# Kernel tuning notes

Hardware: AMD Instinct MI355X
Metric: run time of the kernel (lower is better)

The kernel has to match this reference:

```python
import jax, jax.numpy as jnp
import numpy as np

EMB = 256
N_NODES = 20000
N_EDGES = 200000


def _sage_layer(x, src, dst, edge_attr, W, b, n_nodes):
    # message = x[src] + edge_attr ; mean-aggregate into dst ; ReLU(Linear([x;agg]))
    msg = x[src] + edge_attr                                   # [2E, emb]
    s = jax.ops.segment_sum(msg, dst, num_segments=n_nodes)    # [N, emb]
    cnt = jax.ops.segment_sum(jnp.ones((dst.shape[0], 1), x.dtype), dst,
                              num_segments=n_nodes)            # [N, 1]
    agg = s / jnp.maximum(cnt, 1.0)
    return jax.nn.relu(jnp.concatenate([x, agg], axis=1) @ W + b)


def setup_inputs() -> dict:
    key = jax.random.key(0)
    ks = jax.random.split(key, 12)
    sc = 0.05
    inp = {
        "x": jax.random.normal(ks[0], (N_NODES, EMB), jnp.float32),
        "edge_attr": jax.random.normal(ks[1], (N_EDGES, EMB), jnp.float32),
        "batch_q_embds": jax.random.normal(ks[2], (N_EDGES, EMB), jnp.float32),
        "edge_index": jax.random.randint(ks[3], (2, N_EDGES), 0, N_NODES, jnp.int64
                                         if jax.config.jax_enable_x64 else jnp.int32),
        "W_rev1": jax.random.normal(ks[4], (EMB, EMB), jnp.float32) * sc,
        "b_rev1": jnp.zeros((EMB,), jnp.float32),
        "W_rev2": jax.random.normal(ks[5], (EMB, EMB), jnp.float32) * sc,
        "b_rev2": jnp.zeros((EMB,), jnp.float32),
        "W_sage1": jax.random.normal(ks[6], (2 * EMB, EMB), jnp.float32) * sc,
        "b_sage1": jnp.zeros((EMB,), jnp.float32),
        "W_sage2": jax.random.normal(ks[7], (2 * EMB, EMB), jnp.float32) * sc,
        "b_sage2": jnp.zeros((EMB,), jnp.float32),
        "W_pred1": jax.random.normal(ks[8], (6 * EMB, EMB), jnp.float32) * sc,
        "b_pred1": jnp.zeros((EMB,), jnp.float32),
        "W_pred2": jax.random.normal(ks[9], (EMB, 1), jnp.float32) * sc,
        "b_pred2": jnp.zeros((1,), jnp.float32),
    }
    return inp


def reference(x, edge_attr, batch_q_embds, edge_index,
              W_rev1, b_rev1, W_rev2, b_rev2,
              W_sage1, b_sage1, W_sage2, b_sage2,
              W_pred1, b_pred1, W_pred2, b_pred2):
    src, dst = edge_index[0], edge_index[1]
    # reverse-edge attributes via proj_reverse MLP
    edge_attr_rev = jax.nn.relu(edge_attr @ W_rev1 + b_rev1) @ W_rev2 + b_rev2
    src_f = jnp.concatenate([src, dst])          # [2E]
    dst_f = jnp.concatenate([dst, src])          # [2E]
    ea_f = jnp.concatenate([edge_attr, edge_attr_rev], axis=0)  # [2E, emb]
    # 2-layer GraphSAGE backbone over nodes, collect per-layer outputs
    h1 = _sage_layer(x, src_f, dst_f, ea_f, W_sage1, b_sage1, N_NODES)
    h2 = _sage_layer(h1, src_f, dst_f, ea_f, W_sage2, b_sage2, N_NODES)
    h_e = jnp.concatenate([h1, h2], axis=1)      # [N, 2*emb]
    # per-edge triple features: [q ; h_e[head] ; edge_attr ; h_e[tail]]
    h_triple = jnp.concatenate([batch_q_embds, h_e[src], edge_attr, h_e[dst]], axis=1)
    attn_logits = (jax.nn.relu(h_triple @ W_pred1 + b_pred1) @ W_pred2 + b_pred2)[:, 0]
    # idp-bern sampling (training=True): gumbel-like logistic noise, temp=1
    u = jax.random.uniform(jax.random.key(42), attn_logits.shape,
                           attn_logits.dtype, 1e-10, 1.0 - 1e-10)
    noise = jnp.log(u) - jnp.log(1.0 - u)
    sampled = jax.nn.sigmoid(attn_logits + noise)
    return attn_logits, sampled
```

## Files before the change

kernel.cpp:

```cpp
#include <hip/hip_runtime.h>
#include <cstdint>
#include <cstddef>

#define EMB 256
#define NN 20000
#define NE 200000
#define NE2 400000

typedef unsigned short ushort_t;
typedef __attribute__((ext_vector_type(8))) short bf16x8;
typedef __attribute__((ext_vector_type(4))) float f32x4;

__device__ __forceinline__ ushort_t f2bf(float f) {
    unsigned u = __float_as_uint(f);
    u += 0x7FFFu + ((u >> 16) & 1u);
    return (ushort_t)(u >> 16);
}
__device__ __forceinline__ float bf2f(ushort_t u) {
    return __uint_as_float(((unsigned)u) << 16);
}

__device__ __forceinline__ void async_cp16(const ushort_t* g, ushort_t* l) {
    __builtin_amdgcn_global_load_lds(
        (const __attribute__((address_space(1))) unsigned int*)g,
        (__attribute__((address_space(3))) unsigned int*)l,
        16, 0, 0);
}

__device__ __forceinline__ unsigned rotl32(unsigned v, int d) {
    return (v << d) | (v >> (32 - d));
}
__device__ __forceinline__ void threefry2x32(unsigned k0, unsigned k1,
                                             unsigned x0, unsigned x1,
                                             unsigned& o0, unsigned& o1) {
    unsigned k2 = k0 ^ k1 ^ 0x1BD11BDAu;
    x0 += k0; x1 += k1;
#define TF_R(r) { x0 += x1; x1 = rotl32(x1, (r)); x1 ^= x0; }
    TF_R(13) TF_R(15) TF_R(26) TF_R(6)
    x0 += k1; x1 += k2 + 1u;
    TF_R(17) TF_R(29) TF_R(16) TF_R(24)
    x0 += k2; x1 += k0 + 2u;
    TF_R(13) TF_R(15) TF_R(26) TF_R(6)
    x0 += k0; x1 += k1 + 3u;
    TF_R(17) TF_R(29) TF_R(16) TF_R(24)
    x0 += k1; x1 += k2 + 4u;
    TF_R(13) TF_R(15) TF_R(26) TF_R(6)
    x0 += k2; x1 += k0 + 5u;
#undef TF_R
    o0 = x0; o1 = x1;
}

__global__ void deg_kernel(const int* __restrict__ src, const int* __restrict__ dst,
                           int* __restrict__ deg) {
    int i = blockIdx.x * blockDim.x + threadIdx.x;
    if (i < NE2) {
        int n = (i < NE) ? dst[i] : src[i - NE];
        atomicAdd(&deg[n], 1);
    }
}

__global__ void prefix_kernel(const int* __restrict__ deg, int* __restrict__ row_start,
                              int* __restrict__ cursor) {
    __shared__ int sums[1024];
    int t = threadIdx.x;
    const int CH = (NN + 1023) / 1024;
    int lo = t * CH, hi = lo + CH;
    if (hi > NN) hi = NN;
    if (lo > NN) lo = NN;
    int s = 0;
    for (int n = lo; n < hi; n++) s += deg[n];
    sums[t] = s;
    __syncthreads();
    for (int off = 1; off < 1024; off <<= 1) {
        int v = (t >= off) ? sums[t - off] : 0;
        __syncthreads();
        sums[t] += v;
        __syncthreads();
    }
    int run = (t == 0) ? 0 : sums[t - 1];
    for (int n = lo; n < hi; n++) {
        row_start[n] = run;
        cursor[n] = run;
        run += deg[n];
    }
    if (t == 1023) row_start[NN] = sums[1023];
}

__global__ void scatter_kernel(const int* __restrict__ src, const int* __restrict__ dst,
                               int* __restrict__ cursor, int* __restrict__ elist) {
    int i = blockIdx.x * blockDim.x + threadIdx.x;
    if (i < NE2) {
        int n = (i < NE) ? dst[i] : src[i - NE];
        int pos = atomicAdd(&cursor[n], 1);
        elist[pos] = i;
    }
}

__global__ void conv2_kernel(const float* __restrict__ a, ushort_t* __restrict__ oa, int na8,
                             const float* __restrict__ b, ushort_t* __restrict__ ob, int nb8) {
    int i = blockIdx.x * 256 + threadIdx.x;
    const float* p;
    ushort_t* o;
    if (i < na8) { p = a + (size_t)i * 8; o = oa + (size_t)i * 8; }
    else {
        int j = i - na8;
        if (j >= nb8) return;
        p = b + (size_t)j * 8; o = ob + (size_t)j * 8;
    }
    float4 u = *(const float4*)p;
    float4 v = *(const float4*)(p + 4);
    union { ushort_t s[8]; uint4 w; } r;
    r.s[0] = f2bf(u.x); r.s[1] = f2bf(u.y); r.s[2] = f2bf(u.z); r.s[3] = f2bf(u.w);
    r.s[4] = f2bf(v.x); r.s[5] = f2bf(v.y); r.s[6] = f2bf(v.z); r.s[7] = f2bf(v.w);
    *(uint4*)o = r.w;
}

struct TD { const float* src; ushort_t* dst; int stride, koff, kr; };
struct TA { TD d[8]; };

__global__ void transpose_all_kernel(TA ta) {
    TD t = ta.d[blockIdx.y];
    int k = blockIdx.x;
    if (k >= t.kr) return;
    int n = threadIdx.x;
    t.dst[(size_t)n * t.stride + t.koff + k] = f2bf(t.src[(size_t)k * 256 + n]);
}

template <int KTOT, int EPI, bool A0F32>
__global__ __launch_bounds__(256, 2) void mfma_gemm(
        const void* __restrict__ A0v, int rsA0,
        const ushort_t* __restrict__ A1, int rsA1,
        const ushort_t* __restrict__ Bt, const ushort_t* __restrict__ Bt2,
        const float* __restrict__ bias,
        void* __restrict__ out, void* __restrict__ out2, int rsOut, int M,
        const int* __restrict__ srcp, const int* __restrict__ dstp,
        const float* __restrict__ Hs, const float* __restrict__ Hd,
        const float* __restrict__ w2, const float* __restrict__ b2v,
        float* __restrict__ out_s) {
    __shared__ ushort_t As[128 * 32];
    __shared__ ushort_t Bs[256 * 32];
    __shared__ float red[128];

    int tid = threadIdx.x;
    int lane = tid & 63;
    int wave = tid >> 6;
    int wr = wave >> 1;
    int wc = wave & 1;
    int quad = lane >> 4;
    int col_l = lane & 15;
    int bm = blockIdx.x;

    const ushort_t* Bsel = blockIdx.y ? Bt2 : Bt;
    void* Osel = blockIdx.y ? out2 : out;

    f32x4 acc[4][8];
#pragma unroll
    for (int mt = 0; mt < 4; mt++)
#pragma unroll
        for (int nt = 0; nt < 8; nt++) acc[mt][nt] = (f32x4)0.f;

    for (int k0 = 0; k0 < KTOT; k0 += 32) {
        __syncthreads();
        bool seg1 = (KTOT == 512) && (k0 >= 256);
        if (A0F32 && !seg1) {
#pragma unroll
            for (int j = 0; j < 2; j++) {
                int flat = tid + 256 * j;
                int row = flat >> 2, ch = flat & 3;
                int grow = bm * 128 + row;
                if (grow >= M) grow = M - 1;
                const float* gp = (const float*)A0v + (size_t)grow * rsA0 + k0 + ch * 8;
                float4 u = *(const float4*)gp;
                float4 v = *(const float4*)(gp + 4);
                union { ushort_t s[8]; uint4 w; } r;
                r.s[0] = f2bf(u.x); r.s[1] = f2bf(u.y); r.s[2] = f2bf(u.z); r.s[3] = f2bf(u.w);
                r.s[4] = f2bf(v.x); r.s[5] = f2bf(v.y); r.s[6] = f2bf(v.z); r.s[7] = f2bf(v.w);
                *(uint4*)(As + (size_t)flat * 8) = r.w;
            }
        } else {
            const ushort_t* abase;
            int rs, koffs;
            if (seg1) { abase = A1; rs = rsA1; koffs = k0 - 256; }
            else      { abase = (const ushort_t*)A0v; rs = rsA0; koffs = k0; }
#pragma unroll
            for (int j = 0; j < 2; j++) {
                int flat = tid + 256 * j;
                int row = flat >> 2, ch = flat & 3;
                int grow = bm * 128 + row;
                if (grow >= M) grow = M - 1;
                const ushort_t* gp = abase + (size_t)grow * rs + koffs + ch * 8;
                ushort_t* lp = As + ((wave * 64 + 256 * j) * 8);
                async_cp16(gp, lp);
            }
        }
#pragma unroll
        for (int j = 0; j < 4; j++) {
            int flat = tid + 256 * j;
            int n = flat >> 2, ch = flat & 3;
            const ushort_t* gp = Bsel + (size_t)n * KTOT + k0 + ch * 8;
            ushort_t* lp = Bs + ((wave * 64 + 256 * j) * 8);
            async_cp16(gp, lp);
        }
        __syncthreads();

        bf16x8 a[4], b[8];
#pragma unroll
        for (int mt = 0; mt < 4; mt++)
            a[mt] = *(const bf16x8*)(As + (wr * 64 + mt * 16 + col_l) * 32 + quad * 8);
#pragma unroll
        for (int nt = 0; nt < 8; nt++)
            b[nt] = *(const bf16x8*)(Bs + (wc * 128 + nt * 16 + col_l) * 32 + quad * 8);
#pragma unroll
        for (int mt = 0; mt < 4; mt++)
#pragma unroll
            for (int nt = 0; nt < 8; nt++)
                acc[mt][nt] = __builtin_amdgcn_mfma_f32_16x16x32_bf16(
                    a[mt], b[nt], acc[mt][nt], 0, 0, 0);
    }

    if (EPI == 4) {
        if (tid < 128) red[tid] = 0.f;
        __syncthreads();
        float b1c[8], w2c[8];
#pragma unroll
        for (int nt = 0; nt < 8; nt++) {
            int col = wc * 128 + nt * 16 + col_l;
            b1c[nt] = bias[col];
            w2c[nt] = w2[col];
        }
#pragma unroll
        for (int mt = 0; mt < 4; mt++) {
#pragma unroll
            for (int r = 0; r < 4; r++) {
                int lrow = wr * 64 + mt * 16 + quad * 4 + r;
                int e = bm * 128 + lrow;
                int ec = e < M ? e : M - 1;
                int s = srcp[ec], d = dstp[ec];
                const float* hsr = Hs + (size_t)s * 256;
                const float* hdr = Hd + (size_t)d * 256;
                float part = 0.f;
#pragma unroll
                for (int nt = 0; nt < 8; nt++) {
                    int col = wc * 128 + nt * 16 + col_l;
                    part += fmaxf(acc[mt][nt][r] + hsr[col] + hdr[col] + b1c[nt], 0.f)
                            * w2c[nt];
                }
#pragma unroll
                for (int m = 8; m > 0; m >>= 1) part += __shfl_xor(part, m, 64);
                if (col_l == 0) atomicAdd(&red[lrow], part);
            }
        }
        __syncthreads();
        if (tid < 128) {
            int e = bm * 128 + tid;
            if (e < M) {
                float logit = red[tid] + b2v[0];
                ((float*)out)[e] = logit;
                unsigned y0, y1;
                threefry2x32(0u, 42u, 0u, (unsigned)e, y0, y1);
                unsigned bits = y0 ^ y1;
                float f = __uint_as_float((bits >> 9) | 0x3F800000u) - 1.0f;
                float u = fmaxf(1e-10f, f + 1e-10f);
                float noise = logf(u) - logf(1.0f - u);
                out_s[e] = 1.0f / (1.0f + expf(-(logit + noise)));
            }
        }
        return;
    }

    float bs[8];
    if (EPI >= 2) {
#pragma unroll
        for (int nt = 0; nt < 8; nt++) bs[nt] = bias[wc * 128 + nt * 16 + col_l];
    }
#pragma unroll
    for (int mt = 0; mt < 4; mt++) {
#pragma unroll
        for (int nt = 0; nt < 8; nt++) {
            int colg = wc * 128 + nt * 16 + col_l;
#pragma unroll
            for (int r = 0; r < 4; r++) {
                int rg = bm * 128 + wr * 64 + mt * 16 + quad * 4 + r;
                if (rg < M) {
                    float v = acc[mt][nt][r];
                    if (EPI >= 2) v += bs[nt];
                    if (EPI == 3) v = fmaxf(v, 0.f);
                    if (EPI == 0)
                        ((float*)Osel)[(size_t)rg * rsOut + colg] = v;
                    else
                        ((ushort_t*)Osel)[(size_t)rg * rsOut + colg] = f2bf(v);
                }
            }
        }
    }
}

__global__ __launch_bounds__(64) void agg_bf_kernel(
        const ushort_t* __restrict__ xin, int rsx,
        const ushort_t* __restrict__ eaf, const ushort_t* __restrict__ ear,
        const int* __restrict__ src, const int* __restrict__ dst,
        const int* __restrict__ row_start, const int* __restrict__ elist,
        const int* __restrict__ deg, ushort_t* __restrict__ agg) {
    int n = blockIdx.x;
    int c = threadIdx.x * 4;
    float ax = 0.f, ay = 0.f, az = 0.f, aw = 0.f;
    int beg = row_start[n], end = row_start[n + 1];
    for (int p = beg; p < end; p++) {
        int i = elist[p];
        const ushort_t* xr;
        const ushort_t* er;
        if (i < NE) { xr = xin + (size_t)src[i] * rsx; er = eaf + (size_t)i * 256; }
        else { int j = i - NE; xr = xin + (size_t)dst[j] * rsx; er = ear + (size_t)j * 256; }
        ushort4 xv = *(const ushort4*)(xr + c);
        ushort4 ev = *(const ushort4*)(er + c);
        ax += bf2f(xv.x) + bf2f(ev.x);
        ay += bf2f(xv.y) + bf2f(ev.y);
        az += bf2f(xv.z) + bf2f(ev.z);
        aw += bf2f(xv.w) + bf2f(ev.w);
    }
    float d = fmaxf((float)deg[n], 1.0f);
    ushort4 o;
    o.x = f2bf(ax / d); o.y = f2bf(ay / d); o.z = f2bf(az / d); o.w = f2bf(aw / d);
    *(ushort4*)(agg + (size_t)n * 256 + c) = o;
}

extern "C" void kernel_launch(void* const* d_in, const int* in_sizes, int n_in,
                              void* d_out, int out_size, void* d_ws, size_t ws_size,
                              hipStream_t stream) {
    const float* x        = (const float*)d_in[0];
    const float* ea       = (const float*)d_in[1];
    const float* qemb     = (const float*)d_in[2];
    const int*   eidx     = (const int*)d_in[3];
    const float* W_rev1   = (const float*)d_in[4];
    const float* b_rev1   = (const float*)d_in[5];
    const float* W_rev2   = (const float*)d_in[6];
    const float* b_rev2   = (const float*)d_in[7];
    const float* W_sage1  = (const float*)d_in[8];
    const float* b_sage1  = (const float*)d_in[9];
    const float* W_sage2  = (const float*)d_in[10];
    const float* b_sage2  = (const float*)d_in[11];
    const float* W_pred1  = (const float*)d_in[12];
    const float* b_pred1  = (const float*)d_in[13];
    const float* W_pred2  = (const float*)d_in[14];
    const float* b_pred2  = (const float*)d_in[15];
    float* out = (float*)d_out;

    const int* src = eidx;
    const int* dst = eidx + NE;

    char* w = (char*)d_ws;
    ushort_t* ea_bf  = (ushort_t*)w; w += (size_t)NE * 256 * 2;
    ushort_t* hid_bf = (ushort_t*)w; w += (size_t)NE * 256 * 2;
    ushort_t* ea_rev_bf = (ushort_t*)w; w += (size_t)NE * 256 * 2;
    ushort_t* x_bf   = (ushort_t*)w; w += (size_t)NN * 256 * 2;
    ushort_t* H      = (ushort_t*)w; w += (size_t)NN * 512 * 2;
    ushort_t* agg_bf = (ushort_t*)w; w += (size_t)NN * 256 * 2;
    float*    Hsrc   = (float*)w;    w += (size_t)NN * 256 * 4;
    float*    Hdst   = (float*)w;    w += (size_t)NN * 256 * 4;
    ushort_t* Wt_rev1  = (ushort_t*)w; w += 256 * 256 * 2;
    ushort_t* Wt_rev2  = (ushort_t*)w; w += 256 * 256 * 2;
    ushort_t* Wt_sage1 = (ushort_t*)w; w += 256 * 512 * 2;
    ushort_t* Wt_sage2 = (ushort_t*)w; w += 256 * 512 * 2;
    ushort_t* Wt_src   = (ushort_t*)w; w += 256 * 512 * 2;
    ushort_t* Wt_dst   = (ushort_t*)w; w += 256 * 512 * 2;
    ushort_t* Wt_edge  = (ushort_t*)w; w += 256 * 512 * 2;
    int* deg       = (int*)w; w += (size_t)NN * 4;
    int* row_start = (int*)w; w += (size_t)(NN + 1) * 4;
    int* cursor    = (int*)w; w += (size_t)NN * 4;
    int* elist     = (int*)w; w += (size_t)NE2 * 4;

    const int EB = (NE + 127) / 128;
    const int NB = (NN + 127) / 128;

    hipMemsetAsync(deg, 0, (size_t)NN * 4, stream);
    deg_kernel<<<(NE2 + 255) / 256, 256, 0, stream>>>(src, dst, deg);
    prefix_kernel<<<1, 1024, 0, stream>>>(deg, row_start, cursor);
    scatter_kernel<<<(NE2 + 255) / 256, 256, 0, stream>>>(src, dst, cursor, elist);

    TA ta;
    ta.d[0] = { W_rev1,  Wt_rev1,  256, 0,   256 };
    ta.d[1] = { W_rev2,  Wt_rev2,  256, 0,   256 };
    ta.d[2] = { W_sage1, Wt_sage1, 512, 0,   512 };
    ta.d[3] = { W_sage2, Wt_sage2, 512, 0,   512 };
    ta.d[4] = { W_pred1 + (size_t)256 * 256,  Wt_src,  512, 0,   512 };
    ta.d[5] = { W_pred1 + (size_t)1024 * 256, Wt_dst,  512, 0,   512 };
    ta.d[6] = { W_pred1,                      Wt_edge, 512, 0,   256 };
    ta.d[7] = { W_pred1 + (size_t)768 * 256,  Wt_edge, 512, 256, 256 };
    transpose_all_kernel<<<dim3(512, 8), 256, 0, stream>>>(ta);

    conv2_kernel<<<((NE + NN) * 32 + 255) / 256, 256, 0, stream>>>(
        ea, ea_bf, NE * 32, x, x_bf, NN * 32);

    mfma_gemm<256, 3, false><<<EB, 256, 0, stream>>>(
        ea_bf, 256, nullptr, 0, Wt_rev1, nullptr, b_rev1,
        hid_bf, nullptr, 256, NE, nullptr, nullptr, nullptr, nullptr, nullptr, nullptr, nullptr);
    mfma_gemm<256, 2, false><<<EB, 256, 0, stream>>>(
        hid_bf, 256, nullptr, 0, Wt_rev2, nullptr, b_rev2,
        ea_rev_bf, nullptr, 256, NE, nullptr, nullptr, nullptr, nullptr, nullptr, nullptr, nullptr);

    agg_bf_kernel<<<NN, 64, 0, stream>>>(x_bf, 256, ea_bf, ea_rev_bf,
                                         src, dst, row_start, elist, deg, agg_bf);
    mfma_gemm<512, 3, false><<<NB, 256, 0, stream>>>(
        x_bf, 256, agg_bf, 256, Wt_sage1, nullptr, b_sage1,
        H, nullptr, 512, NN, nullptr, nullptr, nullptr, nullptr, nullptr, nullptr, nullptr);

    agg_bf_kernel<<<NN, 64, 0, stream>>>(H, 512, ea_bf, ea_rev_bf,
                                         src, dst, row_start, elist, deg, agg_bf);
    mfma_gemm<512, 3, false><<<NB, 256, 0, stream>>>(
        H, 512, agg_bf, 256, Wt_sage2, nullptr, b_sage2,
        H + 256, nullptr, 512, NN, nullptr, nullptr, nullptr, nullptr, nullptr, nullptr, nullptr);

    mfma_gemm<512, 0, false><<<dim3(NB, 2), 256, 0, stream>>>(
        H, 512, H + 256, 512, Wt_src, Wt_dst, nullptr,
        Hsrc, Hdst, 256, NN, nullptr, nullptr, nullptr, nullptr, nullptr, nullptr, nullptr);

    mfma_gemm<512, 4, true><<<EB, 256, 0, stream>>>(
        qemb, 256, ea_bf, 256, Wt_edge, nullptr, b_pred1,
        out, nullptr, 0, NE, src, dst, Hsrc, Hdst, W_pred2, b_pred2, out + NE);
}
```

Before: 1.008 ms.

## Double-buffer LDS tiles in MFMA GEMM to overlap loads with compute

```diff
diff --git a/kernel.cpp b/kernel.cpp
--- a/kernel.cpp
+++ b/kernel.cpp
@@ -137,8 +137,8 @@
         const float* __restrict__ Hs, const float* __restrict__ Hd,
         const float* __restrict__ w2, const float* __restrict__ b2v,
         float* __restrict__ out_s) {
-    __shared__ ushort_t As[128 * 32];
-    __shared__ ushort_t Bs[256 * 32];
+    __shared__ ushort_t As[2][128 * 32];
+    __shared__ ushort_t Bs[2][256 * 32];
     __shared__ float red[128];
 
     int tid = threadIdx.x;
@@ -159,25 +159,33 @@
 #pragma unroll
         for (int nt = 0; nt < 8; nt++) acc[mt][nt] = (f32x4)0.f;
 
-    for (int k0 = 0; k0 < KTOT; k0 += 32) {
-        __syncthreads();
+    auto a0_load = [&](int k0, float4* u, float4* v) {
+#pragma unroll
+        for (int j = 0; j < 2; j++) {
+            int flat = tid + 256 * j;
+            int row = flat >> 2, ch = flat & 3;
+            int grow = bm * 128 + row;
+            if (grow >= M) grow = M - 1;
+            const float* gp = (const float*)A0v + (size_t)grow * rsA0 + k0 + ch * 8;
+            u[j] = *(const float4*)gp;
+            v[j] = *(const float4*)(gp + 4);
+        }
+    };
+    auto a0_write = [&](int buf, const float4* u, const float4* v) {
+#pragma unroll
+        for (int j = 0; j < 2; j++) {
+            int flat = tid + 256 * j;
+            union { ushort_t s[8]; uint4 w; } r;
+            r.s[0] = f2bf(u[j].x); r.s[1] = f2bf(u[j].y);
+            r.s[2] = f2bf(u[j].z); r.s[3] = f2bf(u[j].w);
+            r.s[4] = f2bf(v[j].x); r.s[5] = f2bf(v[j].y);
+            r.s[6] = f2bf(v[j].z); r.s[7] = f2bf(v[j].w);
+            *(uint4*)(&As[buf][(size_t)flat * 8]) = r.w;
+        }
+    };
+    auto stage = [&](int buf, int k0, bool skipA) {
         bool seg1 = (KTOT == 512) && (k0 >= 256);
-        if (A0F32 && !seg1) {
-#pragma unroll
-            for (int j = 0; j < 2; j++) {
-                int flat = tid + 256 * j;
-                int row = flat >> 2, ch = flat & 3;
-                int grow = bm * 128 + row;
-                if (grow >= M) grow = M - 1;
-                const float* gp = (const float*)A0v + (size_t)grow * rsA0 + k0 + ch * 8;
-                float4 u = *(const float4*)gp;
-                float4 v = *(const float4*)(gp + 4);
-                union { ushort_t s[8]; uint4 w; } r;
-                r.s[0] = f2bf(u.x); r.s[1] = f2bf(u.y); r.s[2] = f2bf(u.z); r.s[3] = f2bf(u.w);
-                r.s[4] = f2bf(v.x); r.s[5] = f2bf(v.y); r.s[6] = f2bf(v.z); r.s[7] = f2bf(v.w);
-                *(uint4*)(As + (size_t)flat * 8) = r.w;
-            }
-        } else {
+        if (!skipA) {
             const ushort_t* abase;
             int rs, koffs;
             if (seg1) { abase = A1; rs = rsA1; koffs = k0 - 256; }
@@ -189,7 +197,7 @@
                 int grow = bm * 128 + row;
                 if (grow >= M) grow = M - 1;
                 const ushort_t* gp = abase + (size_t)grow * rs + koffs + ch * 8;
-                ushort_t* lp = As + ((wave * 64 + 256 * j) * 8);
+                ushort_t* lp = &As[buf][(wave * 64 + 256 * j) * 8];
                 async_cp16(gp, lp);
             }
         }
@@ -198,24 +206,52 @@
             int flat = tid + 256 * j;
             int n = flat >> 2, ch = flat & 3;
             const ushort_t* gp = Bsel + (size_t)n * KTOT + k0 + ch * 8;
-            ushort_t* lp = Bs + ((wave * 64 + 256 * j) * 8);
+            ushort_t* lp = &Bs[buf][(wave * 64 + 256 * j) * 8];
             async_cp16(gp, lp);
         }
-        __syncthreads();
+    };
+
+    if (A0F32) {
+        float4 u0[2], v0[2];
+        a0_load(0, u0, v0);
+        stage(0, 0, true);
+        a0_write(0, u0, v0);
+    } else {
+        stage(0, 0, false);
+    }
+    __syncthreads();
+
+    const int NIT = KTOT / 32;
+    float4 pu[2], pv[2];
+#pragma unroll 2
+    for (int it = 0; it < NIT; ++it) {
+        int cur = it & 1;
+        int nxt = cur ^ 1;
+        int k1 = (it + 1) * 32;
+        bool do_pref = (it + 1 < NIT);
+        bool seg1_n = (KTOT == 512) && (k1 >= 256);
+        bool pref_f32 = A0F32 && do_pref && !seg1_n;
+
+        if (pref_f32) a0_load(k1, pu, pv);
+        if (do_pref) stage(nxt, k1, pref_f32);
 
         bf16x8 a[4], b[8];
 #pragma unroll
         for (int mt = 0; mt < 4; mt++)
-            a[mt] = *(const bf16x8*)(As + (wr * 64 + mt * 16 + col_l) * 32 + quad * 8);
+            a[mt] = *(const bf16x8*)(&As[cur][(wr * 64 + mt * 16 + col_l) * 32 + quad * 8]);
 #pragma unroll
         for (int nt = 0; nt < 8; nt++)
-            b[nt] = *(const bf16x8*)(Bs + (wc * 128 + nt * 16 + col_l) * 32 + quad * 8);
+            b[nt] = *(const bf16x8*)(&Bs[cur][(wc * 128 + nt * 16 + col_l) * 32 + quad * 8]);
 #pragma unroll
         for (int mt = 0; mt < 4; mt++)
 #pragma unroll
             for (int nt = 0; nt < 8; nt++)
                 acc[mt][nt] = __builtin_amdgcn_mfma_f32_16x16x32_bf16(
                     a[mt], b[nt], acc[mt][nt], 0, 0, 0);
+
+        if (pref_f32) a0_write(nxt, pu, pv);
+
+        __syncthreads();
     }
 
     if (EPI == 4) {
```

Measured after the change: 996.4 us. Within noise of the previous version (-1.2%).

## Triple-buffer GEMM LDS tiles with async prefetch; pre-convert query embeddings to bf16

Applied to the files above, without the earlier changes.

```diff
diff --git a/kernel.cpp b/kernel.cpp
--- a/kernel.cpp
+++ b/kernel.cpp
@@ -25,6 +25,13 @@
         (const __attribute__((address_space(1))) unsigned int*)g,
         (__attribute__((address_space(3))) unsigned int*)l,
         16, 0, 0);
+}
+
+__device__ __forceinline__ void waitbar6() {
+    asm volatile("s_waitcnt vmcnt(6) lgkmcnt(0)\n\ts_barrier" ::: "memory");
+}
+__device__ __forceinline__ void waitbar0() {
+    asm volatile("s_waitcnt vmcnt(0) lgkmcnt(0)\n\ts_barrier" ::: "memory");
 }
 
 __device__ __forceinline__ unsigned rotl32(unsigned v, int d) {
@@ -126,9 +133,9 @@
     t.dst[(size_t)n * t.stride + t.koff + k] = f2bf(t.src[(size_t)k * 256 + n]);
 }
 
-template <int KTOT, int EPI, bool A0F32>
+template <int KTOT, int EPI>
 __global__ __launch_bounds__(256, 2) void mfma_gemm(
-        const void* __restrict__ A0v, int rsA0,
+        const ushort_t* __restrict__ A0, int rsA0,
         const ushort_t* __restrict__ A1, int rsA1,
         const ushort_t* __restrict__ Bt, const ushort_t* __restrict__ Bt2,
         const float* __restrict__ bias,
@@ -137,8 +144,8 @@
         const float* __restrict__ Hs, const float* __restrict__ Hd,
         const float* __restrict__ w2, const float* __restrict__ b2v,
         float* __restrict__ out_s) {
-    __shared__ ushort_t As[128 * 32];
-    __shared__ ushort_t Bs[256 * 32];
+    __shared__ ushort_t As[3][128 * 32];
+    __shared__ ushort_t Bs[3][256 * 32];
     __shared__ float red[128];
 
     int tid = threadIdx.x;
@@ -159,66 +166,60 @@
 #pragma unroll
         for (int nt = 0; nt < 8; nt++) acc[mt][nt] = (f32x4)0.f;
 
-    for (int k0 = 0; k0 < KTOT; k0 += 32) {
-        __syncthreads();
-        bool seg1 = (KTOT == 512) && (k0 >= 256);
-        if (A0F32 && !seg1) {
-#pragma unroll
-            for (int j = 0; j < 2; j++) {
-                int flat = tid + 256 * j;
-                int row = flat >> 2, ch = flat & 3;
-                int grow = bm * 128 + row;
-                if (grow >= M) grow = M - 1;
-                const float* gp = (const float*)A0v + (size_t)grow * rsA0 + k0 + ch * 8;
-                float4 u = *(const float4*)gp;
-                float4 v = *(const float4*)(gp + 4);
-                union { ushort_t s[8]; uint4 w; } r;
-                r.s[0] = f2bf(u.x); r.s[1] = f2bf(u.y); r.s[2] = f2bf(u.z); r.s[3] = f2bf(u.w);
-                r.s[4] = f2bf(v.x); r.s[5] = f2bf(v.y); r.s[6] = f2bf(v.z); r.s[7] = f2bf(v.w);
-                *(uint4*)(As + (size_t)flat * 8) = r.w;
-            }
-        } else {
-            const ushort_t* abase;
-            int rs, koffs;
-            if (seg1) { abase = A1; rs = rsA1; koffs = k0 - 256; }
-            else      { abase = (const ushort_t*)A0v; rs = rsA0; koffs = k0; }
-#pragma unroll
-            for (int j = 0; j < 2; j++) {
-                int flat = tid + 256 * j;
-                int row = flat >> 2, ch = flat & 3;
-                int grow = bm * 128 + row;
-                if (grow >= M) grow = M - 1;
-                const ushort_t* gp = abase + (size_t)grow * rs + koffs + ch * 8;
-                ushort_t* lp = As + ((wave * 64 + 256 * j) * 8);
-                async_cp16(gp, lp);
-            }
+    auto stage = [&](int buf, int k0) {
+        const ushort_t* abase;
+        int rs, koffs;
+        if (KTOT == 512 && k0 >= 256) { abase = A1; rs = rsA1; koffs = k0 - 256; }
+        else                          { abase = A0; rs = rsA0; koffs = k0; }
+#pragma unroll
+        for (int j = 0; j < 2; j++) {
+            int flat = tid + 256 * j;
+            int row = flat >> 2, ch = flat & 3;
+            int grow = bm * 128 + row;
+            if (grow >= M) grow = M - 1;
+            const ushort_t* gp = abase + (size_t)grow * rs + koffs + ch * 8;
+            ushort_t* lp = &As[buf][(wave * 64 + 256 * j) * 8];
+            async_cp16(gp, lp);
         }
 #pragma unroll
         for (int j = 0; j < 4; j++) {
             int flat = tid + 256 * j;
             int n = flat >> 2, ch = flat & 3;
             const ushort_t* gp = Bsel + (size_t)n * KTOT + k0 + ch * 8;
-            ushort_t* lp = Bs + ((wave * 64 + 256 * j) * 8);
+            ushort_t* lp = &Bs[buf][(wave * 64 + 256 * j) * 8];
             async_cp16(gp, lp);
         }
-        __syncthreads();
-
+    };
+
+    auto compute = [&](int buf) {
         bf16x8 a[4], b[8];
 #pragma unroll
         for (int mt = 0; mt < 4; mt++)
-            a[mt] = *(const bf16x8*)(As + (wr * 64 + mt * 16 + col_l) * 32 + quad * 8);
+            a[mt] = *(const bf16x8*)(&As[buf][(wr * 64 + mt * 16 + col_l) * 32 + quad * 8]);
 #pragma unroll
         for (int nt = 0; nt < 8; nt++)
-            b[nt] = *(const bf16x8*)(Bs + (wc * 128 + nt * 16 + col_l) * 32 + quad * 8);
+            b[nt] = *(const bf16x8*)(&Bs[buf][(wc * 128 + nt * 16 + col_l) * 32 + quad * 8]);
 #pragma unroll
         for (int mt = 0; mt < 4; mt++)
 #pragma unroll
             for (int nt = 0; nt < 8; nt++)
                 acc[mt][nt] = __builtin_amdgcn_mfma_f32_16x16x32_bf16(
                     a[mt], b[nt], acc[mt][nt], 0, 0, 0);
-    }
+    };
+
+    const int NIT = KTOT / 32;
+    stage(0, 0);
+    stage(1, 32);
+    for (int k = 0; k < NIT - 1; ++k) {
+        waitbar6();
+        if (k + 2 < NIT) stage((k + 2) % 3, (k + 2) * 32);
+        compute(k % 3);
+    }
+    waitbar0();
+    compute((NIT - 1) % 3);
 
     if (EPI == 4) {
+        __syncthreads();
         if (tid < 128) red[tid] = 0.f;
         __syncthreads();
         float b1c[8], w2c[8];
@@ -391,30 +392,33 @@
     conv2_kernel<<<((NE + NN) * 32 + 255) / 256, 256, 0, stream>>>(
         ea, ea_bf, NE * 32, x, x_bf, NN * 32);
 
-    mfma_gemm<256, 3, false><<<EB, 256, 0, stream>>>(
+    mfma_gemm<256, 3><<<EB, 256, 0, stream>>>(
         ea_bf, 256, nullptr, 0, Wt_rev1, nullptr, b_rev1,
         hid_bf, nullptr, 256, NE, nullptr, nullptr, nullptr, nullptr, nullptr, nullptr, nullptr);
-    mfma_gemm<256, 2, false><<<EB, 256, 0, stream>>>(
+    mfma_gemm<256, 2><<<EB, 256, 0, stream>>>(
         hid_bf, 256, nullptr, 0, Wt_rev2, nullptr, b_rev2,
         ea_rev_bf, nullptr, 256, NE, nullptr, nullptr, nullptr, nullptr, nullptr, nullptr, nullptr);
 
+    conv2_kernel<<<(NE * 32 + 255) / 256, 256, 0, stream>>>(
+        qemb, hid_bf, NE * 32, qemb, hid_bf, 0);
+
     agg_bf_kernel<<<NN, 64, 0, stream>>>(x_bf, 256, ea_bf, ea_rev_bf,
                                          src, dst, row_start, elist, deg, agg_bf);
-    mfma_gemm<512, 3, false><<<NB, 256, 0, stream>>>(
+    mfma_gemm<512, 3><<<NB, 256, 0, stream>>>(
         x_bf, 256, agg_bf, 256, Wt_sage1, nullptr, b_sage1,
         H, nullptr, 512, NN, nullptr, nullptr, nullptr, nullptr, nullptr, nullptr, nullptr);
 
     agg_bf_kernel<<<NN, 64, 0, stream>>>(H, 512, ea_bf, ea_rev_bf,
                                          src, dst, row_start, elist, deg, agg_bf);
-    mfma_gemm<512, 3, false><<<NB, 256, 0, stream>>>(
+    mfma_gemm<512, 3><<<NB, 256, 0, stream>>>(
         H, 512, agg_bf, 256, Wt_sage2, nullptr, b_sage2,
         H + 256, nullptr, 512, NN, nullptr, nullptr, nullptr, nullptr, nullptr, nullptr, nullptr);
 
-    mfma_gemm<512, 0, false><<<dim3(NB, 2), 256, 0, stream>>>(
+    mfma_gemm<512, 0><<<dim3(NB, 2), 256, 0, stream>>>(
         H, 512, H + 256, 512, Wt_src, Wt_dst, nullptr,
         Hsrc, Hdst, 256, NN, nullptr, nullptr, nullptr, nullptr, nullptr, nullptr, nullptr);
 
-    mfma_gemm<512, 4, true><<<EB, 256, 0, stream>>>(
-        qemb, 256, ea_bf, 256, Wt_edge, nullptr, b_pred1,
+    mfma_gemm<512, 4><<<EB, 256, 0, stream>>>(
+        hid_bf, 256, ea_bf, 256, Wt_edge, nullptr, b_pred1,
         out, nullptr, 0, NE, src, dst, Hsrc, Hdst, W_pred2, b_pred2, out + NE);
 }
```

After: 1.086 ms. +7.7%, slower.

## Split GEMM output columns across two blocks and add separate finalize kernel

Applied to the files above, without the earlier changes.

```diff
diff --git a/kernel.cpp b/kernel.cpp
--- a/kernel.cpp
+++ b/kernel.cpp
@@ -126,19 +126,18 @@
     t.dst[(size_t)n * t.stride + t.koff + k] = f2bf(t.src[(size_t)k * 256 + n]);
 }
 
-template <int KTOT, int EPI, bool A0F32>
-__global__ __launch_bounds__(256, 2) void mfma_gemm(
-        const void* __restrict__ A0v, int rsA0,
+template <int KTOT, int EPI>
+__global__ __launch_bounds__(256, 3) void mfma_gemm(
+        const ushort_t* __restrict__ A0, int rsA0,
         const ushort_t* __restrict__ A1, int rsA1,
         const ushort_t* __restrict__ Bt, const ushort_t* __restrict__ Bt2,
         const float* __restrict__ bias,
         void* __restrict__ out, void* __restrict__ out2, int rsOut, int M,
         const int* __restrict__ srcp, const int* __restrict__ dstp,
         const float* __restrict__ Hs, const float* __restrict__ Hd,
-        const float* __restrict__ w2, const float* __restrict__ b2v,
-        float* __restrict__ out_s) {
+        const float* __restrict__ w2) {
     __shared__ ushort_t As[128 * 32];
-    __shared__ ushort_t Bs[256 * 32];
+    __shared__ ushort_t Bs[128 * 32];
     __shared__ float red[128];
 
     int tid = threadIdx.x;
@@ -148,83 +147,69 @@
     int wc = wave & 1;
     int quad = lane >> 4;
     int col_l = lane & 15;
-    int bm = blockIdx.x;
+    int p = blockIdx.x >> 1;
+    int colblk = blockIdx.x & 1;
 
     const ushort_t* Bsel = blockIdx.y ? Bt2 : Bt;
     void* Osel = blockIdx.y ? out2 : out;
 
-    f32x4 acc[4][8];
+    f32x4 acc[4][4];
 #pragma unroll
     for (int mt = 0; mt < 4; mt++)
 #pragma unroll
-        for (int nt = 0; nt < 8; nt++) acc[mt][nt] = (f32x4)0.f;
+        for (int nt = 0; nt < 4; nt++) acc[mt][nt] = (f32x4)0.f;
 
     for (int k0 = 0; k0 < KTOT; k0 += 32) {
         __syncthreads();
-        bool seg1 = (KTOT == 512) && (k0 >= 256);
-        if (A0F32 && !seg1) {
+        {
+            const ushort_t* abase;
+            int rs, koffs;
+            if (KTOT == 512 && k0 >= 256) { abase = A1; rs = rsA1; koffs = k0 - 256; }
+            else                          { abase = A0; rs = rsA0; koffs = k0; }
 #pragma unroll
             for (int j = 0; j < 2; j++) {
                 int flat = tid + 256 * j;
                 int row = flat >> 2, ch = flat & 3;
-                int grow = bm * 128 + row;
-                if (grow >= M) grow = M - 1;
-                const float* gp = (const float*)A0v + (size_t)grow * rsA0 + k0 + ch * 8;
-                float4 u = *(const float4*)gp;
-                float4 v = *(const float4*)(gp + 4);
-                union { ushort_t s[8]; uint4 w; } r;
-                r.s[0] = f2bf(u.x); r.s[1] = f2bf(u.y); r.s[2] = f2bf(u.z); r.s[3] = f2bf(u.w);
-                r.s[4] = f2bf(v.x); r.s[5] = f2bf(v.y); r.s[6] = f2bf(v.z); r.s[7] = f2bf(v.w);
-                *(uint4*)(As + (size_t)flat * 8) = r.w;
-            }
-        } else {
-            const ushort_t* abase;
-            int rs, koffs;
-            if (seg1) { abase = A1; rs = rsA1; koffs = k0 - 256; }
-            else      { abase = (const ushort_t*)A0v; rs = rsA0; koffs = k0; }
-#pragma unroll
-            for (int j = 0; j < 2; j++) {
-                int flat = tid + 256 * j;
-                int row = flat >> 2, ch = flat & 3;
-                int grow = bm * 128 + row;
+                int grow = p * 128 + row;
                 if (grow >= M) grow = M - 1;
                 const ushort_t* gp = abase + (size_t)grow * rs + koffs + ch * 8;
                 ushort_t* lp = As + ((wave * 64 + 256 * j) * 8);
                 async_cp16(gp, lp);
             }
+#pragma unroll
+            for (int j = 0; j < 2; j++) {
+                int flat = tid + 256 * j;
+                int n = flat >> 2, ch = flat & 3;
+                const ushort_t* gp = Bsel + (size_t)(colblk * 128 + n) * KTOT + k0 + ch * 8;
+                ushort_t* lp = Bs + ((wave * 64 + 256 * j) * 8);
+                async_cp16(gp, lp);
+            }
         }
-#pragma unroll
-        for (int j = 0; j < 4; j++) {
-            int flat = tid + 256 * j;
-            int n = flat >> 2, ch = flat & 3;
-            const ushort_t* gp = Bsel + (size_t)n * KTOT + k0 + ch * 8;
-            ushort_t* lp = Bs + ((wave * 64 + 256 * j) * 8);
-            async_cp16(gp, lp);
-        }
-        __syncthreads();
-
-        bf16x8 a[4], b[8];
+        __syncthreads();
+
+        bf16x8 a[4], b[4];
 #pragma unroll
         for (int mt = 0; mt < 4; mt++)
             a[mt] = *(const bf16x8*)(As + (wr * 64 + mt * 16 + col_l) * 32 + quad * 8);
 #pragma unroll
-        for (int nt = 0; nt < 8; nt++)
-            b[nt] = *(const bf16x8*)(Bs + (wc * 128 + nt * 16 + col_l) * 32 + quad * 8);
+        for (int nt = 0; nt < 4; nt++)
+            b[nt] = *(const bf16x8*)(Bs + (wc * 64 + nt * 16 + col_l) * 32 + quad * 8);
 #pragma unroll
         for (int mt = 0; mt < 4; mt++)
 #pragma unroll
-            for (int nt = 0; nt < 8; nt++)
+            for (int nt = 0; nt < 4; nt++)
                 acc[mt][nt] = __builtin_amdgcn_mfma_f32_16x16x32_bf16(
                     a[mt], b[nt], acc[mt][nt], 0, 0, 0);
     }
 
     if (EPI == 4) {
+        __syncthreads();
         if (tid < 128) red[tid] = 0.f;
         __syncthreads();
-        float b1c[8], w2c[8];
-#pragma unroll
-        for (int nt = 0; nt < 8; nt++) {
-            int col = wc * 128 + nt * 16 + col_l;
+        float b1c[4], w2c[4];
+#pragma unroll
+        for (int nt = 0; nt < 4; nt++) {
+            int col = colblk * 128 + wc * 64 + nt * 16 + col_l;
             b1c[nt] = bias[col];
             w2c[nt] = w2[col];
         }
@@ -233,15 +218,15 @@
 #pragma unroll
             for (int r = 0; r < 4; r++) {
                 int lrow = wr * 64 + mt * 16 + quad * 4 + r;
-                int e = bm * 128 + lrow;
+                int e = p * 128 + lrow;
                 int ec = e < M ? e : M - 1;
                 int s = srcp[ec], d = dstp[ec];
                 const float* hsr = Hs + (size_t)s * 256;
                 const float* hdr = Hd + (size_t)d * 256;
                 float part = 0.f;
 #pragma unroll
-                for (int nt = 0; nt < 8; nt++) {
-                    int col = wc * 128 + nt * 16 + col_l;
+                for (int nt = 0; nt < 4; nt++) {
+                    int col = colblk * 128 + wc * 64 + nt * 16 + col_l;
                     part += fmaxf(acc[mt][nt][r] + hsr[col] + hdr[col] + b1c[nt], 0.f)
                             * w2c[nt];
                 }
@@ -252,35 +237,29 @@
         }
         __syncthreads();
         if (tid < 128) {
-            int e = bm * 128 + tid;
+            int e = p * 128 + tid;
             if (e < M) {
-                float logit = red[tid] + b2v[0];
-                ((float*)out)[e] = logit;
-                unsigned y0, y1;
-                threefry2x32(0u, 42u, 0u, (unsigned)e, y0, y1);
-                unsigned bits = y0 ^ y1;
-                float f = __uint_as_float((bits >> 9) | 0x3F800000u) - 1.0f;
-                float u = fmaxf(1e-10f, f + 1e-10f);
-                float noise = logf(u) - logf(1.0f - u);
-                out_s[e] = 1.0f / (1.0f + expf(-(logit + noise)));
+                float* tgt = colblk ? (float*)out2 : (float*)out;
+                tgt[e] = red[tid];
             }
         }
         return;
     }
 
-    float bs[8];
+    float bs[4];
     if (EPI >= 2) {
 #pragma unroll
-        for (int nt = 0; nt < 8; nt++) bs[nt] = bias[wc * 128 + nt * 16 + col_l];
+        for (int nt = 0; nt < 4; nt++)
+            bs[nt] = bias[colblk * 128 + wc * 64 + nt * 16 + col_l];
     }
 #pragma unroll
     for (int mt = 0; mt < 4; mt++) {
 #pragma unroll
-        for (int nt = 0; nt < 8; nt++) {
-            int colg = wc * 128 + nt * 16 + col_l;
+        for (int nt = 0; nt < 4; nt++) {
+            int colg = colblk * 128 + wc * 64 + nt * 16 + col_l;
 #pragma unroll
             for (int r = 0; r < 4; r++) {
-                int rg = bm * 128 + wr * 64 + mt * 16 + quad * 4 + r;
+                int rg = p * 128 + wr * 64 + mt * 16 + quad * 4 + r;
                 if (rg < M) {
                     float v = acc[mt][nt][r];
                     if (EPI >= 2) v += bs[nt];
@@ -293,6 +272,21 @@
             }
         }
     }
+}
+
+__global__ void finalize_kernel(float* __restrict__ out, const float* __restrict__ part1,
+                                const float* __restrict__ b2v, float* __restrict__ out_s) {
+    int e = blockIdx.x * blockDim.x + threadIdx.x;
+    if (e >= NE) return;
+    float logit = out[e] + part1[e] + b2v[0];
+    out[e] = logit;
+    unsigned y0, y1;
+    threefry2x32(0u, 42u, 0u, (unsigned)e, y0, y1);
+    unsigned bits = y0 ^ y1;
+    float f = __uint_as_float((bits >> 9) | 0x3F800000u) - 1.0f;
+    float u = fmaxf(1e-10f, f + 1e-10f);
+    float noise = logf(u) - logf(1.0f - u);
+    out_s[e] = 1.0f / (1.0f + expf(-(logit + noise)));
 }
 
 __global__ __launch_bounds__(64) void agg_bf_kernel(
@@ -357,6 +351,7 @@
     ushort_t* agg_bf = (ushort_t*)w; w += (size_t)NN * 256 * 2;
     float*    Hsrc   = (float*)w;    w += (size_t)NN * 256 * 4;
     float*    Hdst   = (float*)w;    w += (size_t)NN * 256 * 4;
+    float*    part1  = (float*)w;    w += (size_t)NE * 4;
     ushort_t* Wt_rev1  = (ushort_t*)w; w += 256 * 256 * 2;
     ushort_t* Wt_rev2  = (ushort_t*)w; w += 256 * 256 * 2;
     ushort_t* Wt_sage1 = (ushort_t*)w; w += 256 * 512 * 2;
@@ -391,30 +386,35 @@
     conv2_kernel<<<((NE + NN) * 32 + 255) / 256, 256, 0, stream>>>(
         ea, ea_bf, NE * 32, x, x_bf, NN * 32);
 
-    mfma_gemm<256, 3, false><<<EB, 256, 0, stream>>>(
+    mfma_gemm<256, 3><<<EB * 2, 256, 0, stream>>>(
         ea_bf, 256, nullptr, 0, Wt_rev1, nullptr, b_rev1,
-        hid_bf, nullptr, 256, NE, nullptr, nullptr, nullptr, nullptr, nullptr, nullptr, nullptr);
-    mfma_gemm<256, 2, false><<<EB, 256, 0, stream>>>(
+        hid_bf, nullptr, 256, NE, nullptr, nullptr, nullptr, nullptr, nullptr);
+    mfma_gemm<256, 2><<<EB * 2, 256, 0, stream>>>(
         hid_bf, 256, nullptr, 0, Wt_rev2, nullptr, b_rev2,
-        ea_rev_bf, nullptr, 256, NE, nullptr, nullptr, nullptr, nullptr, nullptr, nullptr, nullptr);
+        ea_rev_bf, nullptr, 256, NE, nullptr, nullptr, nullptr, nullptr, nullptr);
+
+    conv2_kernel<<<(NE * 32 + 255) / 256, 256, 0, stream>>>(
+        qemb, hid_bf, NE * 32, qemb, hid_bf, 0);
 
     agg_bf_kernel<<<NN, 64, 0, stream>>>(x_bf, 256, ea_bf, ea_rev_bf,
                                          src, dst, row_start, elist, deg, agg_bf);
-    mfma_gemm<512, 3, false><<<NB, 256, 0, stream>>>(
+    mfma_gemm<512, 3><<<NB * 2, 256, 0, stream>>>(
         x_bf, 256, agg_bf, 256, Wt_sage1, nullptr, b_sage1,
-        H, nullptr, 512, NN, nullptr, nullptr, nullptr, nullptr, nullptr, nullptr, nullptr);
+        H, nullptr, 512, NN, nullptr, nullptr, nullptr, nullptr, nullptr);
 
     agg_bf_kernel<<<NN, 64, 0, stream>>>(H, 512, ea_bf, ea_rev_bf,
                                          src, dst, row_start, elist, deg, agg_bf);
-    mfma_gemm<512, 3, false><<<NB, 256, 0, stream>>>(
+    mfma_gemm<512, 3><<<NB * 2, 256, 0, stream>>>(
         H, 512, agg_bf, 256, Wt_sage2, nullptr, b_sage2,
-        H + 256, nullptr, 512, NN, nullptr, nullptr, nullptr, nullptr, nullptr, nullptr, nullptr);
-
-    mfma_gemm<512, 0, false><<<dim3(NB, 2), 256, 0, stream>>>(
+        H + 256, nullptr, 512, NN, nullptr, nullptr, nullptr, nullptr, nullptr);
+
+    mfma_gemm<512, 0><<<dim3(NB * 2, 2), 256, 0, stream>>>(
         H, 512, H + 256, 512, Wt_src, Wt_dst, nullptr,
-        Hsrc, Hdst, 256, NN, nullptr, nullptr, nullptr, nullptr, nullptr, nullptr, nullptr);
-
-    mfma_gemm<512, 4, true><<<EB, 256, 0, stream>>>(
-        qemb, 256, ea_bf, 256, Wt_edge, nullptr, b_pred1,
-        out, nullptr, 0, NE, src, dst, Hsrc, Hdst, W_pred2, b_pred2, out + NE);
-}
+        Hsrc, Hdst, 256, NN, nullptr, nullptr, nullptr, nullptr, nullptr);
+
+    mfma_gemm<512, 4><<<EB * 2, 256, 0, stream>>>(
+        hid_bf, 256, ea_bf, 256, Wt_edge, nullptr, b_pred1,
+        out, part1, 0, NE, src, dst, Hsrc, Hdst, W_pred2);
+
+    finalize_kernel<<<(NE + 255) / 256, 256, 0, stream>>>(out, part1, b_pred2, out + NE);
+}
```

Result: no change. 1.025 ms (+1.6%).
